# Optimization experiments

Measured on AMD Instinct MI355X. Metric: run time of the kernel, lower is better.

The kernel has to match this reference:

```python
import jax, jax.numpy as jnp
import numpy as np

B, S, E = 32, 1024, 512   # batch, source length, encoder/decoder/attn dim
D, U = 512, 512


def setup_inputs() -> dict:
    key = jax.random.key(0)
    k1, k2, k3, k4, k5 = jax.random.split(key, 5)
    return {
        "outp_enc": jax.random.normal(k1, (B, S, E), dtype=jnp.float32),
        "hidden_dec": jax.random.normal(k2, (B, D), dtype=jnp.float32),
        "Wa": jax.random.normal(k3, (D, U), dtype=jnp.float32) * (1.0 / np.sqrt(D)),
        "Ua": jax.random.normal(k4, (E, U), dtype=jnp.float32) * (1.0 / np.sqrt(E)),
        "Va": jax.random.normal(k5, (U,), dtype=jnp.float32) * (1.0 / np.sqrt(U)),
    }


def reference(outp_enc, hidden_dec, Wa, Ua, Va):
    # Additive (Bahdanau) attention.
    # energies: tanh(Wa h_dec + Ua enc_s) -> [B, S, U]
    dec_proj = hidden_dec @ Wa                      # [B, U]
    enc_proj = jnp.einsum("bse,eu->bsu", outp_enc, Ua)  # [B, S, U]
    e = jnp.tanh(enc_proj + dec_proj[:, None, :])   # [B, S, U]
    scores = jnp.einsum("bsu,u->bs", e, Va)          # [B, S]
    alpha = jax.nn.softmax(scores, axis=-1)          # [B, S]
    context = jnp.einsum("bs,bse->be", alpha, outp_enc)  # [B, E]
    return context
```

## Files before the change

kernel.cpp:

```cpp
#include <hip/hip_runtime.h>
#include <cstdint>
#include <cstddef>

#define BB 32
#define SS 1024
#define EE 512
#define UU 512
#define DD 512

typedef unsigned short ushort_t;
typedef __attribute__((ext_vector_type(8))) short s16x8;
typedef __attribute__((ext_vector_type(8))) _Float16 h16x8;
typedef __attribute__((ext_vector_type(4))) float f32x4;

#define AS1(p) ((const __attribute__((address_space(1))) void*)(const void*)(p))
#define AS3(p) ((__attribute__((address_space(3))) void*)(void*)(p))

__device__ inline float fast_tanh(float x) {
    float ax = fminf(fabsf(x), 20.0f);
    float e2 = __expf(ax * 2.0f);
    float t  = 1.0f - __fdividef(2.0f, e2 + 1.0f);
    return (x < 0.0f) ? -t : t;
}

__global__ void prep_kernel(const float* __restrict__ Ua,
                            const float* __restrict__ hid,
                            const float* __restrict__ Wa,
                            ushort_t* __restrict__ UaSwz,
                            float* __restrict__ decp) {
    __shared__ float sm[256];
    int blk = blockIdx.x, t = threadIdx.x;
    if (blk < 128) {
        int g    = blk * 256 + t;
        int tile = g >> 10;
        int c    = g & 1023;
        int nt = tile >> 3, kt = tile & 7;
        int n = c >> 3, kp = c & 7;
        int ko = kp ^ (n & 7);
        int u  = nt * 128 + n;
        int e0 = kt * 64 + ko * 8;
        s16x8 v;
#pragma unroll
        for (int j = 0; j < 8; ++j) {
            _Float16 h = (_Float16)Ua[(size_t)(e0 + j) * UU + u];
            v[j] = (short)__builtin_bit_cast(unsigned short, h);
        }
        *(s16x8*)(UaSwz + (size_t)g * 8) = v;
    } else {
        int q2 = blk - 128;
        int b = q2 >> 3, q = q2 & 7;
        int uo = t & 63, ch = t >> 6;
        const float* h = hid + (size_t)b * DD;
        float a = 0.f;
        int d0 = ch * 128;
#pragma unroll 4
        for (int d = d0; d < d0 + 128; ++d)
            a = fmaf(h[d], Wa[(size_t)d * UU + q * 64 + uo], a);
        sm[t] = a;
        __syncthreads();
        if (t < 64) {
            float s = sm[t] + sm[64 + t] + sm[128 + t] + sm[192 + t];
            decp[(size_t)b * UU + q * 64 + t] = s;
        }
    }
}

__global__ __launch_bounds__(256, 4)
void scores_kernel(const float* __restrict__ enc,
                   const ushort_t* __restrict__ UaSwz,
                   const float* __restrict__ decp,
                   const float* __restrict__ Va,
                   float* __restrict__ scores) {
    __shared__ __align__(16) ushort_t lds_b[3][128 * 64];
    __shared__ float lds_dv[1024];

    const int tid  = threadIdx.x;
    const int lane = tid & 63;
    const int wave = tid >> 6;
    const int bid  = blockIdx.x;
    const int b    = bid >> 4;
    const int s0   = (bid & 15) * 64;

    lds_dv[tid]       = decp[(size_t)b * UU + tid];
    lds_dv[256 + tid] = decp[(size_t)b * UU + 256 + tid];
    lds_dv[512 + tid] = Va[tid];
    lds_dv[768 + tid] = Va[256 + tid];

    const float* A = enc + ((size_t)b * SS + s0 + wave * 16 + (lane & 15)) * EE
                         + ((lane >> 4) * 8);
    h16x8 a[16];
#pragma unroll
    for (int ks = 0; ks < 16; ++ks) {
        f32x4 v0 = *(const f32x4*)(A + ks * 32);
        f32x4 v1 = *(const f32x4*)(A + ks * 32 + 4);
        h16x8 sh;
#pragma unroll
        for (int j = 0; j < 4; ++j) {
            sh[j]     = (_Float16)v0[j];
            sh[4 + j] = (_Float16)v1[j];
        }
        a[ks] = sh;
    }

    const int nl  = lane & 15;
    const int kq  = lane >> 4;
    const int l7  = lane & 7;
    const int rb  = nl * 64;
    const int kp0 = ((0 + kq) ^ l7) * 8;
    const int kp1 = ((4 + kq) ^ l7) * 8;

#define STAGE(tile, buf)                                                        \
    {                                                                           \
        _Pragma("unroll")                                                       \
        for (int i = 0; i < 4; ++i) {                                           \
            __builtin_amdgcn_global_load_lds(                                   \
                AS1(UaSwz + (size_t)(tile) * 8192 +                             \
                    (((wave * 4 + i) * 64 + lane) * 8)),                        \
                AS3(&lds_b[buf][(wave * 4 + i) * 512]), 16, 0, 0);              \
        }                                                                       \
    }

    float sp0 = 0.f, sp1 = 0.f, sp2 = 0.f, sp3 = 0.f;

    __syncthreads();
    STAGE(0, 0);
    STAGE(1, 1);
    asm volatile("s_waitcnt vmcnt(4)" ::: "memory");
    __builtin_amdgcn_s_barrier();

#pragma unroll
    for (int nt = 0; nt < 4; ++nt) {
        f32x4 acc[8];
#pragma unroll
        for (int nf = 0; nf < 8; ++nf) acc[nf] = f32x4{0.f, 0.f, 0.f, 0.f};

#pragma unroll
        for (int kt = 0; kt < 8; ++kt) {
            const int t8  = nt * 8 + kt;
            const int nxt = (t8 + 2 < 32) ? (t8 + 2) : (t8 + 2 - 32);
            STAGE(nxt, (t8 + 2) % 3);

            const ushort_t* bp = lds_b[t8 % 3];
#pragma unroll
            for (int ks = 0; ks < 2; ++ks) {
                const int kpo = ks ? kp1 : kp0;
#pragma unroll
                for (int nf = 0; nf < 8; ++nf) {
                    h16x8 bh = *(const h16x8*)(bp + nf * 1024 + rb + kpo);
                    acc[nf] = __builtin_amdgcn_mfma_f32_16x16x32_f16(
                        a[kt * 2 + ks], bh, acc[nf], 0, 0, 0);
                }
            }
            asm volatile("s_waitcnt lgkmcnt(0)" ::: "memory");
            asm volatile("s_waitcnt vmcnt(4)" ::: "memory");
            __builtin_amdgcn_s_barrier();
        }

#pragma unroll
        for (int nf = 0; nf < 8; ++nf) {
            int n = nt * 128 + nf * 16 + nl;
            float dp = lds_dv[n];
            float va = lds_dv[512 + n];
            sp0 += fast_tanh(acc[nf][0] + dp) * va;
            sp1 += fast_tanh(acc[nf][1] + dp) * va;
            sp2 += fast_tanh(acc[nf][2] + dp) * va;
            sp3 += fast_tanh(acc[nf][3] + dp) * va;
        }
    }
    asm volatile("s_waitcnt vmcnt(0)" ::: "memory");

#pragma unroll
    for (int off = 1; off < 16; off <<= 1) {
        sp0 += __shfl_xor(sp0, off, 64);
        sp1 += __shfl_xor(sp1, off, 64);
        sp2 += __shfl_xor(sp2, off, 64);
        sp3 += __shfl_xor(sp3, off, 64);
    }
    if (nl == 0) {
        int m = kq * 4;
        float* o = scores + (size_t)b * SS + s0 + wave * 16 + m;
        o[0] = sp0; o[1] = sp1; o[2] = sp2; o[3] = sp3;
    }
#undef STAGE
}

__global__ void context_partial(const float* __restrict__ enc,
                                const float* __restrict__ sc,
                                float* __restrict__ part) {
    __shared__ float red[8];
    __shared__ float al[64];
    int bid = blockIdx.x;
    int b = bid >> 4, scn = bid & 15;
    int t = threadIdx.x, lane = t & 63, wave = t >> 6;

    f32x4 v = *(const f32x4*)(sc + (size_t)b * SS + t * 4);

    float m = fmaxf(fmaxf(v[0], v[1]), fmaxf(v[2], v[3]));
#pragma unroll
    for (int off = 1; off < 64; off <<= 1) m = fmaxf(m, __shfl_xor(m, off, 64));
    if (lane == 0) red[wave] = m;
    __syncthreads();
    m = fmaxf(fmaxf(red[0], red[1]), fmaxf(red[2], red[3]));

    float e0 = __expf(v[0] - m), e1 = __expf(v[1] - m);
    float e2 = __expf(v[2] - m), e3 = __expf(v[3] - m);
    float s = e0 + e1 + e2 + e3;
#pragma unroll
    for (int off = 1; off < 64; off <<= 1) s += __shfl_xor(s, off, 64);
    if (lane == 0) red[4 + wave] = s;
    __syncthreads();
    s = red[4] + red[5] + red[6] + red[7];
    float inv = 1.0f / s;

    if (t >= scn * 16 && t < scn * 16 + 16) {
        int i0 = (t - scn * 16) * 4;
        al[i0 + 0] = e0 * inv; al[i0 + 1] = e1 * inv;
        al[i0 + 2] = e2 * inv; al[i0 + 3] = e3 * inv;
    }
    __syncthreads();

    const float* basep = enc + ((size_t)b * SS + scn * 64) * EE;
    float a0 = 0.f, a1 = 0.f;
#pragma unroll 4
    for (int si = 0; si < 64; ++si) {
        float w = al[si];
        a0 = fmaf(w, basep[(size_t)si * EE + t], a0);
        a1 = fmaf(w, basep[(size_t)si * EE + t + 256], a1);
    }
    float* pp = part + ((size_t)scn * BB + b) * EE;
    pp[t] = a0;
    pp[t + 256] = a1;
}

__global__ void context_reduce(const float* __restrict__ part,
                               float* __restrict__ out) {
    int g = blockIdx.x * 256 + threadIdx.x;
    float s = 0.f;
#pragma unroll
    for (int scn = 0; scn < 16; ++scn) s += part[(size_t)scn * BB * EE + g];
    out[g] = s;
}

extern "C" void kernel_launch(void* const* d_in, const int* in_sizes, int n_in,
                              void* d_out, int out_size, void* d_ws, size_t ws_size,
                              hipStream_t stream) {
    const float* enc = (const float*)d_in[0];
    const float* hid = (const float*)d_in[1];
    const float* Wa  = (const float*)d_in[2];
    const float* Ua  = (const float*)d_in[3];
    const float* Va  = (const float*)d_in[4];
    float* out = (float*)d_out;

    char* ws = (char*)d_ws;
    float*    decp   = (float*)(ws);
    float*    scores = (float*)(ws + 65536);
    float*    part   = (float*)(ws + 196608);
    ushort_t* UaSwz  = (ushort_t*)(ws + 1245184);

    prep_kernel<<<384, 256, 0, stream>>>(Ua, hid, Wa, UaSwz, decp);
    scores_kernel<<<512, 256, 0, stream>>>(enc, UaSwz, decp, Va, scores);
    context_partial<<<512, 256, 0, stream>>>(enc, scores, part);
    context_reduce<<<64, 256, 0, stream>>>(part, out);
}
```

Before: 69.50 us.

## Give each scores wave two 16-row A tiles to reuse B fragments

The scores kernel now runs 2 waves per block instead of 4. Each wave handles 32 source rows held as two register-resident fp16 A tiles, and every Ua fragment read from LDS feeds two MFMAs. This halves LDS B-fragment reads per MFMA and the barrier count per unit of work. In exchange it roughly doubles accumulator and A-register pressure, lowers threads per block, and changes launch bounds to (128,1), which may reduce occupancy and latency hiding.

```diff
diff --git a/kernel.cpp b/kernel.cpp
--- a/kernel.cpp
+++ b/kernel.cpp
@@ -65,13 +65,13 @@
     }
 }
 
-__global__ __launch_bounds__(256, 4)
+__global__ __launch_bounds__(128, 1)
 void scores_kernel(const float* __restrict__ enc,
                    const ushort_t* __restrict__ UaSwz,
                    const float* __restrict__ decp,
                    const float* __restrict__ Va,
                    float* __restrict__ scores) {
-    __shared__ __align__(16) ushort_t lds_b[3][128 * 64];
+    __shared__ __align__(16) ushort_t lds_b[3][8192];
     __shared__ float lds_dv[1024];
 
     const int tid  = threadIdx.x;
@@ -81,26 +81,12 @@
     const int b    = bid >> 4;
     const int s0   = (bid & 15) * 64;
 
-    lds_dv[tid]       = decp[(size_t)b * UU + tid];
-    lds_dv[256 + tid] = decp[(size_t)b * UU + 256 + tid];
-    lds_dv[512 + tid] = Va[tid];
-    lds_dv[768 + tid] = Va[256 + tid];
-
-    const float* A = enc + ((size_t)b * SS + s0 + wave * 16 + (lane & 15)) * EE
-                         + ((lane >> 4) * 8);
-    h16x8 a[16];
-#pragma unroll
-    for (int ks = 0; ks < 16; ++ks) {
-        f32x4 v0 = *(const f32x4*)(A + ks * 32);
-        f32x4 v1 = *(const f32x4*)(A + ks * 32 + 4);
-        h16x8 sh;
-#pragma unroll
-        for (int j = 0; j < 4; ++j) {
-            sh[j]     = (_Float16)v0[j];
-            sh[4 + j] = (_Float16)v1[j];
-        }
-        a[ks] = sh;
-    }
+#pragma unroll
+    for (int j = 0; j < 4; ++j)
+        lds_dv[j * 128 + tid] = decp[(size_t)b * UU + j * 128 + tid];
+#pragma unroll
+    for (int j = 0; j < 4; ++j)
+        lds_dv[512 + j * 128 + tid] = Va[j * 128 + tid];
 
     const int nl  = lane & 15;
     const int kq  = lane >> 4;
@@ -109,30 +95,54 @@
     const int kp0 = ((0 + kq) ^ l7) * 8;
     const int kp1 = ((4 + kq) ^ l7) * 8;
 
+    const float* A0 = enc + ((size_t)b * SS + s0 + wave * 32 + nl) * EE + kq * 8;
+    h16x8 a0[16], a1[16];
+#pragma unroll
+    for (int ks = 0; ks < 16; ++ks) {
+        f32x4 v0 = *(const f32x4*)(A0 + ks * 32);
+        f32x4 v1 = *(const f32x4*)(A0 + ks * 32 + 4);
+        f32x4 w0 = *(const f32x4*)(A0 + 16 * EE + ks * 32);
+        f32x4 w1 = *(const f32x4*)(A0 + 16 * EE + ks * 32 + 4);
+        h16x8 x, y;
+#pragma unroll
+        for (int j = 0; j < 4; ++j) {
+            x[j]     = (_Float16)v0[j];
+            x[4 + j] = (_Float16)v1[j];
+            y[j]     = (_Float16)w0[j];
+            y[4 + j] = (_Float16)w1[j];
+        }
+        a0[ks] = x;
+        a1[ks] = y;
+    }
+
 #define STAGE(tile, buf)                                                        \
     {                                                                           \
         _Pragma("unroll")                                                       \
-        for (int i = 0; i < 4; ++i) {                                           \
+        for (int i = 0; i < 8; ++i) {                                           \
             __builtin_amdgcn_global_load_lds(                                   \
                 AS1(UaSwz + (size_t)(tile) * 8192 +                             \
-                    (((wave * 4 + i) * 64 + lane) * 8)),                        \
-                AS3(&lds_b[buf][(wave * 4 + i) * 512]), 16, 0, 0);              \
+                    ((i * 128 + wave * 64 + lane) * 8)),                        \
+                AS3(&lds_b[buf][(i * 128 + wave * 64) * 8]), 16, 0, 0);         \
         }                                                                       \
     }
 
-    float sp0 = 0.f, sp1 = 0.f, sp2 = 0.f, sp3 = 0.f;
+    f32x4 sp0 = {0.f, 0.f, 0.f, 0.f};
+    f32x4 sp1 = {0.f, 0.f, 0.f, 0.f};
 
     __syncthreads();
     STAGE(0, 0);
     STAGE(1, 1);
-    asm volatile("s_waitcnt vmcnt(4)" ::: "memory");
+    asm volatile("s_waitcnt vmcnt(8)" ::: "memory");
     __builtin_amdgcn_s_barrier();
 
 #pragma unroll
     for (int nt = 0; nt < 4; ++nt) {
-        f32x4 acc[8];
-#pragma unroll
-        for (int nf = 0; nf < 8; ++nf) acc[nf] = f32x4{0.f, 0.f, 0.f, 0.f};
+        f32x4 acc0[8], acc1[8];
+#pragma unroll
+        for (int nf = 0; nf < 8; ++nf) {
+            acc0[nf] = f32x4{0.f, 0.f, 0.f, 0.f};
+            acc1[nf] = f32x4{0.f, 0.f, 0.f, 0.f};
+        }
 
 #pragma unroll
         for (int kt = 0; kt < 8; ++kt) {
@@ -147,12 +157,14 @@
 #pragma unroll
                 for (int nf = 0; nf < 8; ++nf) {
                     h16x8 bh = *(const h16x8*)(bp + nf * 1024 + rb + kpo);
-                    acc[nf] = __builtin_amdgcn_mfma_f32_16x16x32_f16(
-                        a[kt * 2 + ks], bh, acc[nf], 0, 0, 0);
+                    acc0[nf] = __builtin_amdgcn_mfma_f32_16x16x32_f16(
+                        a0[kt * 2 + ks], bh, acc0[nf], 0, 0, 0);
+                    acc1[nf] = __builtin_amdgcn_mfma_f32_16x16x32_f16(
+                        a1[kt * 2 + ks], bh, acc1[nf], 0, 0, 0);
                 }
             }
             asm volatile("s_waitcnt lgkmcnt(0)" ::: "memory");
-            asm volatile("s_waitcnt vmcnt(4)" ::: "memory");
+            asm volatile("s_waitcnt vmcnt(8)" ::: "memory");
             __builtin_amdgcn_s_barrier();
         }
 
@@ -161,25 +173,31 @@
             int n = nt * 128 + nf * 16 + nl;
             float dp = lds_dv[n];
             float va = lds_dv[512 + n];
-            sp0 += fast_tanh(acc[nf][0] + dp) * va;
-            sp1 += fast_tanh(acc[nf][1] + dp) * va;
-            sp2 += fast_tanh(acc[nf][2] + dp) * va;
-            sp3 += fast_tanh(acc[nf][3] + dp) * va;
+#pragma unroll
+            for (int r = 0; r < 4; ++r) {
+                sp0[r] += fast_tanh(acc0[nf][r] + dp) * va;
+                sp1[r] += fast_tanh(acc1[nf][r] + dp) * va;
+            }
         }
     }
     asm volatile("s_waitcnt vmcnt(0)" ::: "memory");
 
 #pragma unroll
     for (int off = 1; off < 16; off <<= 1) {
-        sp0 += __shfl_xor(sp0, off, 64);
-        sp1 += __shfl_xor(sp1, off, 64);
-        sp2 += __shfl_xor(sp2, off, 64);
-        sp3 += __shfl_xor(sp3, off, 64);
+#pragma unroll
+        for (int r = 0; r < 4; ++r) {
+            sp0[r] += __shfl_xor(sp0[r], off, 64);
+            sp1[r] += __shfl_xor(sp1[r], off, 64);
+        }
     }
     if (nl == 0) {
-        int m = kq * 4;
-        float* o = scores + (size_t)b * SS + s0 + wave * 16 + m;
-        o[0] = sp0; o[1] = sp1; o[2] = sp2; o[3] = sp3;
+        float* o0 = scores + (size_t)b * SS + s0 + wave * 32 + kq * 4;
+        float* o1 = o0 + 16;
+#pragma unroll
+        for (int r = 0; r < 4; ++r) {
+            o0[r] = sp0[r];
+            o1[r] = sp1[r];
+        }
     }
 #undef STAGE
 }
@@ -258,7 +276,7 @@
     ushort_t* UaSwz  = (ushort_t*)(ws + 1245184);
 
     prep_kernel<<<384, 256, 0, stream>>>(Ua, hid, Wa, UaSwz, decp);
-    scores_kernel<<<512, 256, 0, stream>>>(enc, UaSwz, decp, Va, scores);
+    scores_kernel<<<512, 128, 0, stream>>>(enc, UaSwz, decp, Va, scores);
     context_partial<<<512, 256, 0, stream>>>(enc, scores, part);
     context_reduce<<<64, 256, 0, stream>>>(part, out);
 }
```

Result: slower. 84.85 us (+22.1%).

## Shrink scores blocks to two waves over 32 rows with double-buffered Ua staging

Applied to the files above, without the earlier changes.

The scores kernel now runs 1024 blocks of 128 threads, each covering 32 source rows instead of 64, and switches the Ua tile ring from triple to double buffering with a full vmcnt(0) wait per k-step. The intent is more blocks and less LDS per block for better occupancy and load balance across CUs. In exchange, each Ua tile is streamed from global/L2 twice as often per row of output, the prefetch depth drops to one tile so load latency is less hidden, and launch bounds now say 1 block per CU.

```diff
diff --git a/kernel.cpp b/kernel.cpp
--- a/kernel.cpp
+++ b/kernel.cpp
@@ -65,42 +65,28 @@
     }
 }
 
-__global__ __launch_bounds__(256, 4)
+__global__ __launch_bounds__(128, 1)
 void scores_kernel(const float* __restrict__ enc,
                    const ushort_t* __restrict__ UaSwz,
                    const float* __restrict__ decp,
                    const float* __restrict__ Va,
                    float* __restrict__ scores) {
-    __shared__ __align__(16) ushort_t lds_b[3][128 * 64];
+    __shared__ __align__(16) ushort_t lds_b[2][8192];
     __shared__ float lds_dv[1024];
 
     const int tid  = threadIdx.x;
     const int lane = tid & 63;
     const int wave = tid >> 6;
     const int bid  = blockIdx.x;
-    const int b    = bid >> 4;
-    const int s0   = (bid & 15) * 64;
-
-    lds_dv[tid]       = decp[(size_t)b * UU + tid];
-    lds_dv[256 + tid] = decp[(size_t)b * UU + 256 + tid];
-    lds_dv[512 + tid] = Va[tid];
-    lds_dv[768 + tid] = Va[256 + tid];
-
-    const float* A = enc + ((size_t)b * SS + s0 + wave * 16 + (lane & 15)) * EE
-                         + ((lane >> 4) * 8);
-    h16x8 a[16];
-#pragma unroll
-    for (int ks = 0; ks < 16; ++ks) {
-        f32x4 v0 = *(const f32x4*)(A + ks * 32);
-        f32x4 v1 = *(const f32x4*)(A + ks * 32 + 4);
-        h16x8 sh;
-#pragma unroll
-        for (int j = 0; j < 4; ++j) {
-            sh[j]     = (_Float16)v0[j];
-            sh[4 + j] = (_Float16)v1[j];
-        }
-        a[ks] = sh;
-    }
+    const int b    = bid >> 5;
+    const int s0   = (bid & 31) * 32;
+
+#pragma unroll
+    for (int j = 0; j < 4; ++j)
+        lds_dv[j * 128 + tid] = decp[(size_t)b * UU + j * 128 + tid];
+#pragma unroll
+    for (int j = 0; j < 4; ++j)
+        lds_dv[512 + j * 128 + tid] = Va[j * 128 + tid];
 
     const int nl  = lane & 15;
     const int kq  = lane >> 4;
@@ -109,23 +95,37 @@
     const int kp0 = ((0 + kq) ^ l7) * 8;
     const int kp1 = ((4 + kq) ^ l7) * 8;
 
+    const float* A = enc + ((size_t)b * SS + s0 + wave * 16 + nl) * EE + kq * 8;
+    h16x8 a[16];
+#pragma unroll
+    for (int ks = 0; ks < 16; ++ks) {
+        f32x4 v0 = *(const f32x4*)(A + ks * 32);
+        f32x4 v1 = *(const f32x4*)(A + ks * 32 + 4);
+        h16x8 sh;
+#pragma unroll
+        for (int j = 0; j < 4; ++j) {
+            sh[j]     = (_Float16)v0[j];
+            sh[4 + j] = (_Float16)v1[j];
+        }
+        a[ks] = sh;
+    }
+
 #define STAGE(tile, buf)                                                        \
     {                                                                           \
         _Pragma("unroll")                                                       \
-        for (int i = 0; i < 4; ++i) {                                           \
+        for (int i = 0; i < 8; ++i) {                                           \
             __builtin_amdgcn_global_load_lds(                                   \
                 AS1(UaSwz + (size_t)(tile) * 8192 +                             \
-                    (((wave * 4 + i) * 64 + lane) * 8)),                        \
-                AS3(&lds_b[buf][(wave * 4 + i) * 512]), 16, 0, 0);              \
+                    ((i * 128 + wave * 64 + lane) * 8)),                        \
+                AS3(&lds_b[buf][(i * 128 + wave * 64) * 8]), 16, 0, 0);         \
         }                                                                       \
     }
 
-    float sp0 = 0.f, sp1 = 0.f, sp2 = 0.f, sp3 = 0.f;
+    f32x4 sp = {0.f, 0.f, 0.f, 0.f};
 
     __syncthreads();
     STAGE(0, 0);
-    STAGE(1, 1);
-    asm volatile("s_waitcnt vmcnt(4)" ::: "memory");
+    asm volatile("s_waitcnt vmcnt(0)" ::: "memory");
     __builtin_amdgcn_s_barrier();
 
 #pragma unroll
@@ -136,11 +136,10 @@
 
 #pragma unroll
         for (int kt = 0; kt < 8; ++kt) {
-            const int t8  = nt * 8 + kt;
-            const int nxt = (t8 + 2 < 32) ? (t8 + 2) : (t8 + 2 - 32);
-            STAGE(nxt, (t8 + 2) % 3);
-
-            const ushort_t* bp = lds_b[t8 % 3];
+            const int t8 = nt * 8 + kt;
+            if (t8 < 31) STAGE(t8 + 1, (t8 + 1) & 1);
+
+            const ushort_t* bp = lds_b[t8 & 1];
 #pragma unroll
             for (int ks = 0; ks < 2; ++ks) {
                 const int kpo = ks ? kp1 : kp0;
@@ -152,7 +151,7 @@
                 }
             }
             asm volatile("s_waitcnt lgkmcnt(0)" ::: "memory");
-            asm volatile("s_waitcnt vmcnt(4)" ::: "memory");
+            asm volatile("s_waitcnt vmcnt(0)" ::: "memory");
             __builtin_amdgcn_s_barrier();
         }
 
@@ -161,25 +160,22 @@
             int n = nt * 128 + nf * 16 + nl;
             float dp = lds_dv[n];
             float va = lds_dv[512 + n];
-            sp0 += fast_tanh(acc[nf][0] + dp) * va;
-            sp1 += fast_tanh(acc[nf][1] + dp) * va;
-            sp2 += fast_tanh(acc[nf][2] + dp) * va;
-            sp3 += fast_tanh(acc[nf][3] + dp) * va;
-        }
-    }
-    asm volatile("s_waitcnt vmcnt(0)" ::: "memory");
+#pragma unroll
+            for (int r = 0; r < 4; ++r)
+                sp[r] += fast_tanh(acc[nf][r] + dp) * va;
+        }
+    }
 
 #pragma unroll
     for (int off = 1; off < 16; off <<= 1) {
-        sp0 += __shfl_xor(sp0, off, 64);
-        sp1 += __shfl_xor(sp1, off, 64);
-        sp2 += __shfl_xor(sp2, off, 64);
-        sp3 += __shfl_xor(sp3, off, 64);
+#pragma unroll
+        for (int r = 0; r < 4; ++r)
+            sp[r] += __shfl_xor(sp[r], off, 64);
     }
     if (nl == 0) {
-        int m = kq * 4;
-        float* o = scores + (size_t)b * SS + s0 + wave * 16 + m;
-        o[0] = sp0; o[1] = sp1; o[2] = sp2; o[3] = sp3;
+        float* o = scores + (size_t)b * SS + s0 + wave * 16 + kq * 4;
+#pragma unroll
+        for (int r = 0; r < 4; ++r) o[r] = sp[r];
     }
 #undef STAGE
 }
@@ -258,7 +254,7 @@
     ushort_t* UaSwz  = (ushort_t*)(ws + 1245184);
 
     prep_kernel<<<384, 256, 0, stream>>>(Ua, hid, Wa, UaSwz, decp);
-    scores_kernel<<<512, 256, 0, stream>>>(enc, UaSwz, decp, Va, scores);
+    scores_kernel<<<1024, 128, 0, stream>>>(enc, UaSwz, decp, Va, scores);
     context_partial<<<512, 256, 0, stream>>>(enc, scores, part);
     context_reduce<<<64, 256, 0, stream>>>(part, out);
 }
```

Measured after the change: 77.71 us. 1.12x slower.
